# Performance work log

Hardware: AMD Instinct MI355X
Metric: run time of the kernel (lower is better)

Reference implementation:

```python
import jax, jax.numpy as jnp
import numpy as np

B, S, D, H = 4, 2048, 1024, 16
DK = D // H


def setup_inputs() -> dict:
    key = jax.random.key(0)
    ks = jax.random.split(key, 5)
    init_std = np.sqrt(2.0 / (D + D))  # trunc bound proxy; plain randn clamped below
    trunc = 3 * init_std

    def w(k):
        return jnp.clip(jax.random.normal(k, (D, D), dtype=jnp.float32), -trunc, trunc)

    x = jax.random.normal(ks[0], (B, S, D), dtype=jnp.float32)
    return {
        "x": x,
        "W_Q": w(ks[1]),
        "W_K": w(ks[2]),
        "W_V": w(ks[3]),
        "W_O": w(ks[4]),
        "is_causal": 1,
    }


def reference(x, W_Q, W_K, W_V, W_O, is_causal):
    b, s, d = x.shape
    # Linear: y = W @ x with W:[out,in], x:[..., in]
    def proj(W, t):
        y = jnp.einsum("oi,bsi->bso", W, t)
        # [b, s, h*dk] -> [b, h, s, dk]
        return y.reshape(b, s, H, DK).transpose(0, 2, 1, 3)

    q = proj(W_Q, x)
    k = proj(W_K, x)
    v = proj(W_V, x)

    scores = jnp.einsum("bhqd,bhkd->bhqk", q, k) * (DK ** -0.5)
    if is_causal:
        causal = jnp.tril(jnp.ones((s, s), dtype=bool))
        scores = jnp.where(causal, scores, -jnp.inf)
    attn = jax.nn.softmax(scores, axis=-1)
    out = jnp.einsum("bhqk,bhkd->bhqd", attn, v)
    out = out.transpose(0, 2, 1, 3).reshape(b, s, H * DK)
    return jnp.einsum("oi,bsi->bso", W_O, out)
```

## Files before the change

### kernel.cpp

```cpp
#include <hip/hip_runtime.h>
#include <stdint.h>

#define NB 4
#define NS 2048
#define ND 1024
#define NH 16
#define NDK 64
#define L2E 1.44269504088896340736f
#define AS1 __attribute__((address_space(1)))
#define AS3 __attribute__((address_space(3)))

typedef __attribute__((ext_vector_type(8)))  short     s16x8;
typedef __attribute__((ext_vector_type(4)))  float     f32x4;
typedef __attribute__((ext_vector_type(16))) float     f32x16;
typedef __attribute__((ext_vector_type(4)))  unsigned  u32x4;

__device__ __forceinline__ unsigned short f2bf(float f) {
    union { float f; unsigned u; } v; v.f = f;
    unsigned r = v.u + 0x7FFFu + ((v.u >> 16) & 1u);
    return (unsigned short)(r >> 16);
}
__device__ __forceinline__ unsigned cvt_pk_bf16(float lo, float hi) {
    unsigned r;
    asm("v_cvt_pk_bf16_f32 %0, %1, %2" : "=v"(r) : "v"(lo), "v"(hi));
    return r;
}
__device__ __forceinline__ void pl32swap(unsigned &a, unsigned &b) {
    asm volatile("v_permlane32_swap_b32 %0, %1" : "+v"(a), "+v"(b));
}
__device__ __forceinline__ float exp2_hw(float x) {
    float r; asm("v_exp_f32 %0, %1" : "=v"(r) : "v"(x)); return r;
}
__device__ __forceinline__ f32x16 fz16() {
    f32x16 z;
#pragma unroll
    for (int r = 0; r < 16; ++r) z[r] = 0.f;
    return z;
}
__device__ __forceinline__ f32x16 mfma32(const s16x8& a, const s16x8& b, const f32x16& c) {
    return __builtin_amdgcn_mfma_f32_32x32x16_bf16(a, b, c, 0, 0, 0);
}

__global__ void convert_all(const void* __restrict__ x,  const void* __restrict__ wq,
                            const void* __restrict__ wk, const void* __restrict__ wv,
                            unsigned short* __restrict__ XB, unsigned short* __restrict__ WQKV,
                            int* __restrict__ flag) {
    __shared__ int sfl;
    int tid = threadIdx.x;
    if (tid < 64) {
        int cnt = 0;
        const unsigned* xw = (const unsigned*)x;
        for (int i = tid; i < 1024; i += 64) {
            unsigned lo = xw[i] & 0xFFFFu;
            unsigned e  = (lo >> 7) & 0xFFu;
            cnt += (e >= 100u && e <= 140u) ? 1 : 0;
        }
        for (int d = 1; d < 64; d <<= 1) cnt += __shfl_xor(cnt, d);
        if (tid == 0) {
            sfl = (cnt > 512) ? 1 : 0;
            if (blockIdx.x == 0) flag[0] = sfl;
        }
    }
    __syncthreads();
    int fl = sfl;

    const int A  = (NB * NS * ND) / 8;
    const int WC = (ND * ND) / 8;
    int i = blockIdx.x * blockDim.x + tid;
    int stride = gridDim.x * blockDim.x;
    int total = A + 3 * WC;
    for (; i < total; i += stride) {
        const void* src; unsigned short* dst; long o8;
        if (i < A) { src = x; dst = XB; o8 = i; }
        else {
            int k = i - A, which = k >> 17, o = k & (WC - 1);
            src = which == 0 ? wq : (which == 1 ? wk : wv);
            dst = WQKV + (long)which * (ND * ND);
            o8 = o;
        }
        u32x4 v;
        if (fl) {
            v = *(const u32x4*)((const unsigned short*)src + o8 * 8);
        } else {
            const float* p = (const float*)src + o8 * 8;
            f32x4 a = *(const f32x4*)p;
            f32x4 b = *(const f32x4*)(p + 4);
            v[0] = cvt_pk_bf16(a[0], a[1]);
            v[1] = cvt_pk_bf16(a[2], a[3]);
            v[2] = cvt_pk_bf16(b[0], b[1]);
            v[3] = cvt_pk_bf16(b[2], b[3]);
        }
        *(u32x4*)(dst + o8 * 8) = v;
    }
}

__global__ void convert_bf16(const void* __restrict__ src, unsigned short* __restrict__ dst,
                             int n8, const int* __restrict__ flagp) {
    int i = blockIdx.x * blockDim.x + threadIdx.x;
    int stride = gridDim.x * blockDim.x;
    int fl = *flagp;
    for (; i < n8; i += stride) {
        u32x4 v;
        if (fl) {
            v = *(const u32x4*)((const unsigned short*)src + (long)i * 8);
        } else {
            const float* p = (const float*)src + (long)i * 8;
            f32x4 a = *(const f32x4*)p;
            f32x4 b = *(const f32x4*)(p + 4);
            v[0] = cvt_pk_bf16(a[0], a[1]);
            v[1] = cvt_pk_bf16(a[2], a[3]);
            v[2] = cvt_pk_bf16(b[0], b[1]);
            v[3] = cvt_pk_bf16(b[2], b[3]);
        }
        *(u32x4*)(dst + (long)i * 8) = v;
    }
}

__device__ __forceinline__ void stage_glds64(const unsigned short* __restrict__ src, int ld,
                                             long r0, int k0, unsigned short* lds, int tid) {
#pragma unroll
    for (int h = 0; h < 4; ++h) {
        int c = h * 256 + tid;
        int row = c >> 3;
        int scol = (c & 7) ^ (row & 7);
        const unsigned short* gp = src + (r0 + row) * ld + k0 + scol * 8;
        unsigned short* lp = lds + (c & ~63) * 8;
        __builtin_amdgcn_global_load_lds(
            (const AS1 unsigned short*)gp, (AS3 unsigned short*)lp, 16, 0, 0);
    }
}

template<int OUT_MODE, int NXB>
__global__ __launch_bounds__(256, 2)
void gemm3(const unsigned short* __restrict__ A, const unsigned short* __restrict__ W,
           void* __restrict__ dst, const int* __restrict__ flagp, float scale)
{
    __shared__ unsigned short As[128 * 64];
    __shared__ unsigned short Bs[128 * 64];
    const long TOKc = (long)NB * NS * ND;
    int tid  = threadIdx.x;
    int w    = tid >> 6, lane = tid & 63;
    int wr   = w >> 1,   wc   = w & 1;
    int nwg = (int)(gridDim.x * gridDim.y);
    int bid = (int)(blockIdx.y * gridDim.x + blockIdx.x);
    int nb  = (bid & 7) * (nwg >> 3) + (bid >> 3);
    int n0  = (nb % NXB) * 128;
    long m0 = (long)(nb / NXB) * 128;
    int fl  = *flagp;

    f32x4 zero4 = {0.f, 0.f, 0.f, 0.f};
    f32x4 acc[4][4];
#pragma unroll
    for (int i = 0; i < 4; ++i)
#pragma unroll
        for (int j = 0; j < 4; ++j) acc[i][j] = zero4;

    int lr = lane & 15, lg = lane >> 4;

    for (int k0 = 0; k0 < 1024; k0 += 64) {
        __syncthreads();
        stage_glds64(A, 1024, m0, k0, As, tid);
        stage_glds64(W, 1024, n0, k0, Bs, tid);
        __syncthreads();
#pragma unroll
        for (int kk = 0; kk < 2; ++kk) {
            s16x8 af[4], bf[4];
#pragma unroll
            for (int i = 0; i < 4; ++i) {
                int row = wr * 64 + i * 16 + lr;
                int u = (kk * 4 + lg) ^ (lr & 7);
                af[i] = *(const s16x8*)(As + row * 64 + u * 8);
            }
#pragma unroll
            for (int j = 0; j < 4; ++j) {
                int row = wc * 64 + j * 16 + lr;
                int u = (kk * 4 + lg) ^ (lr & 7);
                bf[j] = *(const s16x8*)(Bs + row * 64 + u * 8);
            }
#pragma unroll
            for (int i = 0; i < 4; ++i)
#pragma unroll
                for (int j = 0; j < 4; ++j)
                    acc[i][j] = __builtin_amdgcn_mfma_f32_16x16x32_bf16(af[i], bf[j], acc[i][j], 0, 0, 0);
        }
    }

    int rbase = (lane >> 4) * 4;
#pragma unroll
    for (int i = 0; i < 4; ++i)
#pragma unroll
        for (int j = 0; j < 4; ++j)
#pragma unroll
            for (int r = 0; r < 4; ++r) {
                long m = m0 + wr * 64 + i * 16 + rbase + r;
                int  n = n0 + wc * 64 + j * 16 + lr;
                float v = acc[i][j][r];
                if (OUT_MODE == 3) {
                    long b = m >> 11, s = m & 2047;
                    int hh = (n >> 6) & 15, dk = n & 63;
                    float sc = (n < 1024) ? scale : 1.0f;
                    long off = (n >= 1024) ? TOKc : 0;
                    ((unsigned short*)dst)[off + (((b * NH + hh) * NS) + s) * NDK + dk] = f2bf(v * sc);
                } else if (OUT_MODE == 1) {
                    int hh = (int)(m >> 6), dk = (int)(m & 63);
                    long b = n >> 11, s = n & 2047;
                    ((unsigned short*)dst)[(((b * NH + hh) * NDK) + dk) * NS + s] = f2bf(v * scale);
                } else {
                    if (fl) ((unsigned short*)dst)[m * 1024 + n] = f2bf(v * scale);
                    else    ((float*)dst)[m * 1024 + n] = v * scale;
                }
            }
}

__device__ __forceinline__ void stage_tile64(const char* __restrict__ srcbase, int rowstride,
                                             unsigned short* lds, int tid) {
#pragma unroll
    for (int h = 0; h < 2; ++h) {
        int c = h * 256 + tid;
        int L = c * 16;
        int row = L >> 7;
        int sr  = (L & 127) ^ ((row & 7) << 4);
        const char* gp = srcbase + row * rowstride + sr;
        unsigned short* lp = lds + (c & ~63) * 8;
        __builtin_amdgcn_global_load_lds((const AS1 unsigned short*)gp,
                                         (AS3 unsigned short*)lp, 16, 0, 0);
    }
}

__device__ __forceinline__ void sm64s(f32x16& st0, f32x16& st1,
                                      bool mask, int kv0, int qb, int l31, int hi,
                                      s16x8* pf)
{
    if (mask) {
        int q = qb + l31;
#pragma unroll
        for (int r = 0; r < 16; ++r) {
            int crow = (r & 3) + 8 * (r >> 2) + 4 * hi;
            if (kv0 + crow > q)      st0[r] = -1e30f;
            if (kv0 + 32 + crow > q) st1[r] = -1e30f;
        }
    }
#pragma unroll
    for (int r = 0; r < 16; ++r) {
        st0[r] = exp2_hw(st0[r]);
        st1[r] = exp2_hw(st1[r]);
    }
#pragma unroll
    for (int half = 0; half < 2; ++half) {
        const f32x16& st = half ? st1 : st0;
        unsigned b0 = cvt_pk_bf16(st[0],  st[1]);
        unsigned b1 = cvt_pk_bf16(st[2],  st[3]);
        unsigned b2 = cvt_pk_bf16(st[4],  st[5]);
        unsigned b3 = cvt_pk_bf16(st[6],  st[7]);
        unsigned b4 = cvt_pk_bf16(st[8],  st[9]);
        unsigned b5 = cvt_pk_bf16(st[10], st[11]);
        unsigned b6 = cvt_pk_bf16(st[12], st[13]);
        unsigned b7 = cvt_pk_bf16(st[14], st[15]);
        pl32swap(b0, b2);  pl32swap(b1, b3);
        pl32swap(b4, b6);  pl32swap(b5, b7);
        union { unsigned u[4]; s16x8 v; } p0, p1;
        p0.u[0] = b0; p0.u[1] = b1; p0.u[2] = b2; p0.u[3] = b3;
        p1.u[0] = b4; p1.u[1] = b5; p1.u[2] = b6; p1.u[3] = b7;
        pf[half * 2]     = p0.v;
        pf[half * 2 + 1] = p1.v;
    }
}

__device__ __forceinline__ void attn_epi(unsigned short* epb, const f32x16& o0, const f32x16& o1,
                                         float lsum, int l31, int hi, int lane,
                                         unsigned short* __restrict__ Oo, int qb, int b, int hh)
{
    float inv = 1.0f / lsum;
#pragma unroll
    for (int j = 0; j < 2; ++j) {
        const f32x16& o = j ? o1 : o0;
#pragma unroll
        for (int g = 0; g < 4; ++g) {
            int d0 = j * 32 + g * 8 + hi * 4;
            unsigned lo = cvt_pk_bf16(o[g * 4 + 0] * inv, o[g * 4 + 1] * inv);
            unsigned hw = cvt_pk_bf16(o[g * 4 + 2] * inv, o[g * 4 + 3] * inv);
            unsigned short* p = epb + l31 * 72 + d0;
            *(unsigned*)(p)     = lo;
            *(unsigned*)(p + 2) = hw;
        }
    }
    asm volatile("s_waitcnt lgkmcnt(0)" ::: "memory");
    __builtin_amdgcn_sched_barrier(0);
#pragma unroll
    for (int rr = 0; rr < 4; ++rr) {
        int q2 = rr * 8 + (lane >> 3);
        int d2 = (lane & 7) * 8;
        u32x4 vv = *(const u32x4*)(epb + q2 * 72 + d2);
        *(u32x4*)(Oo + (((long)b * NS + qb + q2) * ND) + hh * NDK + d2) = vv;
    }
}

__global__ __launch_bounds__(256, 3)
void attn_fwd14(const unsigned short* __restrict__ Q,
                const unsigned short* __restrict__ Kt,
                const unsigned short* __restrict__ Vt,
                unsigned short* __restrict__ Oo,
                const int* __restrict__ causalp)
{
    __shared__ char lds[2][16384];
    int tid = threadIdx.x, w = tid >> 6, lane = tid & 63;
    int l31 = lane & 31, hi = lane >> 5;
    int bh = blockIdx.x;
    int j  = 15 - (int)blockIdx.y;
    int t  = 4 * j + w, qb = t * 32;
    int causal = *causalp;
    int nst   = causal ? (2 * j + 2) : (NS / 64);
    int sdiag = causal ? (t >> 1) : 0x7FFFFFFF;

    const unsigned short* Qh = Q  + bh * (NS * NDK);
    const char* Khb = (const char*)(Kt + (long)bh * NS * NDK);
    const char* Vhb = (const char*)(Vt + (long)bh * NDK * NS);

    s16x8 qf[4];
#pragma unroll
    for (int kd = 0; kd < 4; ++kd)
        qf[kd] = *(const s16x8*)(Qh + (qb + l31) * NDK + kd * 16 + hi * 8);

    s16x8 onesv;
#pragma unroll
    for (int i = 0; i < 8; ++i) onesv[i] = (short)0x3F80;

    int koff[4];
#pragma unroll
    for (int kd = 0; kd < 4; ++kd)
        koff[kd] = l31 * 128 + ((kd * 32 + hi * 16) ^ ((l31 & 7) << 4));

    const f32x16 Z16 = fz16();
    f32x16 o0 = fz16(), o1 = fz16(), o2 = fz16();

    stage_tile64(Khb, 128, (unsigned short*)&lds[0][0], tid);
    stage_tile64(Vhb, NS * 2, (unsigned short*)&lds[0][8192], tid);
    __syncthreads();

    int cur = 0;
    for (int s = 0; s < nst; ++s) {
        if (s + 1 < nst) {
            int kv1 = (s + 1) * 64;
            stage_tile64(Khb + (long)kv1 * 128, 128, (unsigned short*)&lds[cur ^ 1][0], tid);
            stage_tile64(Vhb + kv1 * 2, NS * 2, (unsigned short*)&lds[cur ^ 1][8192], tid);
        }
        if (s <= sdiag) {
            const char* kb = &lds[cur][0];
            const char* vb = &lds[cur][8192];
            f32x16 st0, st1;
            __builtin_amdgcn_s_setprio(1);
            {
                s16x8 k0 = *(const s16x8*)(kb + koff[0]);
                s16x8 k1 = *(const s16x8*)(kb + 4096 + koff[0]);
                st0 = mfma32(k0, qf[0], Z16);
                st1 = mfma32(k1, qf[0], Z16);
            }
#pragma unroll
            for (int kd = 1; kd < 4; ++kd) {
                s16x8 k0 = *(const s16x8*)(kb + koff[kd]);
                s16x8 k1 = *(const s16x8*)(kb + 4096 + koff[kd]);
                st0 = mfma32(k0, qf[kd], st0);
                st1 = mfma32(k1, qf[kd], st1);
            }
            __builtin_amdgcn_s_setprio(0);
            s16x8 pf[4];
            sm64s(st0, st1, s == sdiag, s * 64, qb, l31, hi, pf);
            __builtin_amdgcn_s_setprio(1);
#pragma unroll
            for (int ks = 0; ks < 4; ++ks) {
                s16x8 va = *(const s16x8*)(vb + koff[ks]);
                s16x8 wb = *(const s16x8*)(vb + 4096 + koff[ks]);
                o0 = mfma32(va, pf[ks], o0);
                o1 = mfma32(wb, pf[ks], o1);
                o2 = mfma32(onesv, pf[ks], o2);
            }
            __builtin_amdgcn_s_setprio(0);
        }
        __syncthreads();
        cur ^= 1;
    }

    unsigned short* ep = (unsigned short*)&lds[0][0] + w * (32 * 72);
    attn_epi(ep, o0, o1, o2[0], l31, hi, lane, Oo, qb, bh >> 4, bh & 15);
}

extern "C" void kernel_launch(void* const* d_in, const int* in_sizes, int n_in,
                              void* d_out, int out_size, void* d_ws, size_t ws_size,
                              hipStream_t stream) {
    const void* x  = d_in[0];
    const void* Wq = d_in[1];
    const void* Wk = d_in[2];
    const void* Wv = d_in[3];
    const void* Wo = d_in[4];
    const int* causal = (const int*)d_in[5];

    const long TOK  = (long)NB * NS * ND;
    const long WTOK = (long)ND * ND;
    size_t need = 256 + 4UL * TOK * 2;
    if (ws_size < need) return;

    char* ws = (char*)d_ws;
    int* flag = (int*)ws;
    unsigned short* Qb = (unsigned short*)(ws + 256);
    unsigned short* Kb = Qb + TOK;
    unsigned short* Vb = Kb + TOK;
    unsigned short* XB = Vb + TOK;
    unsigned short* Ab = XB;
    unsigned short* WOB = Qb;
    unsigned short* WQKV = (unsigned short*)((char*)d_out + (size_t)out_size * 2 - 3UL * WTOK * 2);

    convert_all<<<2048, 256, 0, stream>>>(x, Wq, Wk, Wv, XB, WQKV, flag);

    dim3 blk(256);
    gemm3<3, 16><<<dim3(16, 64), blk, 0, stream>>>(XB, WQKV, Qb, flag, 0.125f * L2E);
    gemm3<1, 64><<<dim3(64, 8), blk, 0, stream>>>(WQKV + 2 * WTOK, XB, Vb, flag, 1.0f);
    attn_fwd14<<<dim3(64, 16), blk, 0, stream>>>(Qb, Kb, Vb, Ab, causal);
    convert_bf16<<<512, 256, 0, stream>>>(Wo, WOB, (int)(WTOK / 8), flag);
    gemm3<2, 8><<<dim3(8, 64), blk, 0, stream>>>(Ab, WOB, d_out, flag, 1.0f);
}
```

Measured before the change: 152.4 us.

## Split long causal attention query tiles across KV halves with merge kernel

```diff
diff --git a/kernel.cpp b/kernel.cpp
--- a/kernel.cpp
+++ b/kernel.cpp
@@ -296,21 +296,30 @@
 }
 
 __global__ __launch_bounds__(256, 3)
-void attn_fwd14(const unsigned short* __restrict__ Q,
+void attn_fwd16(const unsigned short* __restrict__ Q,
                 const unsigned short* __restrict__ Kt,
                 const unsigned short* __restrict__ Vt,
                 unsigned short* __restrict__ Oo,
-                const int* __restrict__ causalp)
+                const int* __restrict__ causalp,
+                float* __restrict__ Po, float* __restrict__ Lo, int variant)
 {
     __shared__ char lds[2][16384];
+    static const signed char TJ1[22] = {9,8,15,15,7,14,14,6,13,13,12,12,5,11,11,10,10,4,3,2,1,0};
+    static const signed char TH1[22] = {-1,-1,0,1,-1,0,1,-1,0,1,0,1,-1,0,1,0,1,-1,-1,-1,-1,-1};
     int tid = threadIdx.x, w = tid >> 6, lane = tid & 63;
     int l31 = lane & 31, hi = lane >> 5;
     int bh = blockIdx.x;
-    int j  = 15 - (int)blockIdx.y;
+    int y  = blockIdx.y;
+    int j, hf;
+    if (variant) { j = TJ1[y]; hf = TH1[y]; }
+    else         { j = 15 - y; hf = -1; }
     int t  = 4 * j + w, qb = t * 32;
     int causal = *causalp;
-    int nst   = causal ? (2 * j + 2) : (NS / 64);
-    int sdiag = causal ? (t >> 1) : 0x7FFFFFFF;
+    int sdw = t >> 1;
+    int mid = causal ? j : 15;
+    int lo  = (hf == 1) ? (mid + 1) : 0;
+    int hiW = causal ? ((hf == 0) ? j : sdw)       : ((hf == 0) ? 15 : 31);
+    int hiB = causal ? ((hf == 0) ? j : 2 * j + 1) : ((hf == 0) ? 15 : 31);
 
     const unsigned short* Qh = Q  + bh * (NS * NDK);
     const char* Khb = (const char*)(Kt + (long)bh * NS * NDK);
@@ -333,18 +342,18 @@
     const f32x16 Z16 = fz16();
     f32x16 o0 = fz16(), o1 = fz16(), o2 = fz16();
 
-    stage_tile64(Khb, 128, (unsigned short*)&lds[0][0], tid);
-    stage_tile64(Vhb, NS * 2, (unsigned short*)&lds[0][8192], tid);
+    stage_tile64(Khb + (long)lo * 64 * 128, 128, (unsigned short*)&lds[0][0], tid);
+    stage_tile64(Vhb + (long)lo * 64 * 2, NS * 2, (unsigned short*)&lds[0][8192], tid);
     __syncthreads();
 
     int cur = 0;
-    for (int s = 0; s < nst; ++s) {
-        if (s + 1 < nst) {
-            int kv1 = (s + 1) * 64;
-            stage_tile64(Khb + (long)kv1 * 128, 128, (unsigned short*)&lds[cur ^ 1][0], tid);
+    for (int s = lo; s <= hiB; ++s) {
+        if (s < hiB) {
+            long kv1 = (long)(s + 1) * 64;
+            stage_tile64(Khb + kv1 * 128, 128, (unsigned short*)&lds[cur ^ 1][0], tid);
             stage_tile64(Vhb + kv1 * 2, NS * 2, (unsigned short*)&lds[cur ^ 1][8192], tid);
         }
-        if (s <= sdiag) {
+        if (s <= hiW) {
             const char* kb = &lds[cur][0];
             const char* vb = &lds[cur][8192];
             f32x16 st0, st1;
@@ -364,7 +373,7 @@
             }
             __builtin_amdgcn_s_setprio(0);
             s16x8 pf[4];
-            sm64s(st0, st1, s == sdiag, s * 64, qb, l31, hi, pf);
+            sm64s(st0, st1, causal && (s == sdw), s * 64, qb, l31, hi, pf);
             __builtin_amdgcn_s_setprio(1);
 #pragma unroll
             for (int ks = 0; ks < 4; ++ks) {
@@ -380,8 +389,58 @@
         cur ^= 1;
     }
 
-    unsigned short* ep = (unsigned short*)&lds[0][0] + w * (32 * 72);
-    attn_epi(ep, o0, o1, o2[0], l31, hi, lane, Oo, qb, bh >> 4, bh & 15);
+    if (hf < 0) {
+        unsigned short* ep = (unsigned short*)&lds[0][0] + w * (32 * 72);
+        attn_epi(ep, o0, o1, o2[0], l31, hi, lane, Oo, qb, bh >> 4, bh & 15);
+    } else {
+        int st = t - 40;
+        long idx = (((long)hf * 64 + bh) * 24 + st);
+        float* po = Po + idx * 2048;
+#pragma unroll
+        for (int r = 0; r < 16; ++r) {
+            int crow = (r & 3) + 8 * (r >> 2) + 4 * hi;
+            po[crow * 32 + l31]        = o0[r];
+            po[(32 + crow) * 32 + l31] = o1[r];
+        }
+        if (hi == 0) Lo[idx * 32 + l31] = o2[0];
+    }
+}
+
+__global__ __launch_bounds__(256)
+void attn_merge(const float* __restrict__ Po, const float* __restrict__ Lo,
+                unsigned short* __restrict__ Oo)
+{
+    __shared__ float T[64 * 33];
+    __shared__ float Ls[32];
+    int tid = threadIdx.x;
+    int st = blockIdx.x % 24, bh = blockIdx.x / 24;
+    long i0 = (((long)0 * 64 + bh) * 24 + st);
+    long i1 = (((long)1 * 64 + bh) * 24 + st);
+    const float* p0 = Po + i0 * 2048;
+    const float* p1 = Po + i1 * 2048;
+    int i = tid * 8;
+    f32x4 a0 = *(const f32x4*)(p0 + i);
+    f32x4 a1 = *(const f32x4*)(p0 + i + 4);
+    f32x4 b0 = *(const f32x4*)(p1 + i);
+    f32x4 b1 = *(const f32x4*)(p1 + i + 4);
+    int d = i >> 5, q = i & 31;
+    float* row = T + d * 33 + q;
+    row[0] = a0[0] + b0[0]; row[1] = a0[1] + b0[1];
+    row[2] = a0[2] + b0[2]; row[3] = a0[3] + b0[3];
+    row[4] = a1[0] + b1[0]; row[5] = a1[1] + b1[1];
+    row[6] = a1[2] + b1[2]; row[7] = a1[3] + b1[3];
+    if (tid < 32) Ls[tid] = Lo[i0 * 32 + tid] + Lo[i1 * 32 + tid];
+    __syncthreads();
+    int q2 = tid >> 3, dg = (tid & 7) * 8;
+    float inv = 1.0f / Ls[q2];
+    unsigned outw[4];
+#pragma unroll
+    for (int k = 0; k < 4; ++k)
+        outw[k] = cvt_pk_bf16(T[(dg + 2 * k) * 33 + q2] * inv,
+                              T[(dg + 2 * k + 1) * 33 + q2] * inv);
+    int b = bh >> 4, hh = bh & 15;
+    long qg = (long)(st + 40) * 32 + q2;
+    *(u32x4*)(Oo + ((long)b * NS + qg) * ND + hh * NDK + dg) = *(u32x4*)outw;
 }
 
 extern "C" void kernel_launch(void* const* d_in, const int* in_sizes, int n_in,
@@ -396,8 +455,12 @@
 
     const long TOK  = (long)NB * NS * ND;
     const long WTOK = (long)ND * ND;
-    size_t need = 256 + 4UL * TOK * 2;
+    const long PO_FLOATS = 2L * 64 * 24 * 2048;
+    const long LO_FLOATS = 2L * 64 * 24 * 32;
+    size_t need  = 256 + 4UL * TOK * 2;
+    size_t need2 = need + (size_t)(PO_FLOATS + LO_FLOATS) * 4 + 256;
     if (ws_size < need) return;
+    int variant = (ws_size >= need2) ? 1 : 0;
 
     char* ws = (char*)d_ws;
     int* flag = (int*)ws;
@@ -407,6 +470,8 @@
     unsigned short* XB = Vb + TOK;
     unsigned short* Ab = XB;
     unsigned short* WOB = Qb;
+    float* Po = (float*)(ws + ((need + 255) & ~(size_t)255));
+    float* Lo = Po + PO_FLOATS;
     unsigned short* WQKV = (unsigned short*)((char*)d_out + (size_t)out_size * 2 - 3UL * WTOK * 2);
 
     convert_all<<<2048, 256, 0, stream>>>(x, Wq, Wk, Wv, XB, WQKV, flag);
@@ -414,7 +479,9 @@
     dim3 blk(256);
     gemm3<3, 16><<<dim3(16, 64), blk, 0, stream>>>(XB, WQKV, Qb, flag, 0.125f * L2E);
     gemm3<1, 64><<<dim3(64, 8), blk, 0, stream>>>(WQKV + 2 * WTOK, XB, Vb, flag, 1.0f);
-    attn_fwd14<<<dim3(64, 16), blk, 0, stream>>>(Qb, Kb, Vb, Ab, causal);
+    attn_fwd16<<<dim3(64, variant ? 22 : 16), blk, 0, stream>>>(Qb, Kb, Vb, Ab, causal,
+                                                                Po, Lo, variant);
+    if (variant) attn_merge<<<dim3(24 * 64), blk, 0, stream>>>(Po, Lo, Ab);
     convert_bf16<<<512, 256, 0, stream>>>(Wo, WOB, (int)(WTOK / 8), flag);
     gemm3<2, 8><<<dim3(8, 64), blk, 0, stream>>>(Ab, WOB, d_out, flag, 1.0f);
 }
```

New measurement: 159.8 us. 1.05x slower.
